# Kernel tuning notes

Hardware: AMD Instinct MI355X
Metric: run time of the kernel (lower is better)

Reference implementation:

```python
import jax, jax.numpy as jnp
import numpy as np

N = 12                      # input_size / Cholesky matrix dim
TRI = N * (N + 1) // 2      # 78 = MLP output size (lower-tri element count)
LW = 32                     # layer_width (hardcoded in source)
BATCH = 262144


def setup_inputs() -> dict:
    key = jax.random.key(0)
    ks = jax.random.split(key, 7)
    s = lambda fan_in: 1.0 / np.sqrt(fan_in)  # torch Linear default init scale
    return {
        "x":  jax.random.normal(ks[0], (BATCH, N), dtype=jnp.float32),
        "W1": jax.random.uniform(ks[1], (4 * LW, N),   minval=-s(N),      maxval=s(N),      dtype=jnp.float32),
        "b1": jax.random.uniform(ks[2], (4 * LW,),     minval=-s(N),      maxval=s(N),      dtype=jnp.float32),
        "W2": jax.random.uniform(ks[3], (LW, 4 * LW),  minval=-s(4 * LW), maxval=s(4 * LW), dtype=jnp.float32),
        "b2": jax.random.uniform(ks[4], (LW,),         minval=-s(4 * LW), maxval=s(4 * LW), dtype=jnp.float32),
        "W3": jax.random.uniform(ks[5], (TRI, LW),     minval=-s(LW),     maxval=s(LW),     dtype=jnp.float32),
        "b3": jax.random.uniform(ks[6], (TRI,),        minval=-s(LW),     maxval=s(LW),     dtype=jnp.float32),
    }


def reference(x, W1, b1, W2, b2, W3, b3):
    # MLP: Linear -> ELU -> Linear -> ELU -> Linear -> Softplus
    h = jax.nn.elu(x @ W1.T + b1)
    h = jax.nn.elu(h @ W2.T + b2)
    v = jax.nn.softplus(h @ W3.T + b3)          # [B, TRI]
    # Scatter tri elements into lower triangle, row-major (i>=j) order,
    # matching the source's nested i,j loop == jnp.tril_indices ordering.
    rows, cols = jnp.tril_indices(N)
    B = v.shape[0]
    L = jnp.zeros((B, N, N), dtype=v.dtype).at[:, rows, cols].set(v)
    # M @ M^T (batched), SPD output
    return jnp.einsum("bij,bkj->bik", L, L)
```

## Files before the change

kernel.cpp:

```cpp
#include <hip/hip_runtime.h>
#include <math.h>


namespace {

constexpr int ND  = 12;
constexpr int TRI = 78;
constexpr int BLK = 256;
constexpr int SPB = 512;

constexpr int oW3    = 0;
constexpr int oB3    = 2496;
constexpr int oW1    = 2576;
constexpr int oB1    = 4112;
constexpr int oW2T   = 4240;
constexpr int oB2    = 8336;
constexpr int oStage = 2576;
constexpr int STRIDE = 148;
constexpr int LDSF   = oStage + 64 * STRIDE;

__device__ __forceinline__ float elu_f(float v) {
    return v > 0.0f ? v : __expf(v) - 1.0f;
}
__device__ __forceinline__ float softplus_f(float v) {
    return fmaxf(v, 0.0f) + __logf(1.0f + __expf(-fabsf(v)));
}

__global__ __launch_bounds__(BLK, 2) void qnc(
    const float* __restrict__ x,
    const float* __restrict__ W1, const float* __restrict__ b1,
    const float* __restrict__ W2, const float* __restrict__ b2,
    const float* __restrict__ W3, const float* __restrict__ b3,
    float* __restrict__ out)
{
    __shared__ float lds[LDSF];
    const int t = threadIdx.x;

    for (int i = t; i < 2496; i += BLK) lds[oW3 + i] = W3[i];
    for (int i = t; i < 78;   i += BLK) lds[oB3 + i] = b3[i];
    for (int i = t; i < 1536; i += BLK) lds[oW1 + i] = W1[i];
    for (int i = t; i < 128;  i += BLK) lds[oB1 + i] = b1[i];
    for (int i = t; i < 4096; i += BLK) lds[oW2T + i] = W2[(i & 31) * 128 + (i >> 5)];
    for (int i = t; i < 32;   i += BLK) lds[oB2 + i] = b2[i];
    __syncthreads();

    const long sbase = (long)blockIdx.x * SPB;

    float xv0[ND], xv1[ND];
    {
        const float4* p0 = (const float4*)(x + (sbase + t) * ND);
        const float4* p1 = (const float4*)(x + (sbase + 256 + t) * ND);
        float4 a, b, c;
        a = p0[0]; b = p0[1]; c = p0[2];
        xv0[0]=a.x; xv0[1]=a.y; xv0[2]=a.z; xv0[3]=a.w;
        xv0[4]=b.x; xv0[5]=b.y; xv0[6]=b.z; xv0[7]=b.w;
        xv0[8]=c.x; xv0[9]=c.y; xv0[10]=c.z; xv0[11]=c.w;
        a = p1[0]; b = p1[1]; c = p1[2];
        xv1[0]=a.x; xv1[1]=a.y; xv1[2]=a.z; xv1[3]=a.w;
        xv1[4]=b.x; xv1[5]=b.y; xv1[6]=b.z; xv1[7]=b.w;
        xv1[8]=c.x; xv1[9]=c.y; xv1[10]=c.z; xv1[11]=c.w;
    }

    float h20[32], h21[32];
    #pragma unroll
    for (int k = 0; k < 32; ++k) { h20[k] = 0.0f; h21[k] = 0.0f; }

    #pragma unroll 2
    for (int j = 0; j < 128; ++j) {
        const float4 wa = *(const float4*)&lds[oW1 + j*12];
        const float4 wb = *(const float4*)&lds[oW1 + j*12 + 4];
        const float4 wc = *(const float4*)&lds[oW1 + j*12 + 8];
        const float bj = lds[oB1 + j];

        float p0 = fmaf(xv0[0], wa.x, bj);
        float p1 = xv0[1] * wa.y;
        float p2 = xv0[2] * wa.z;
        float p3 = xv0[3] * wa.w;
        p0 = fmaf(xv0[4], wb.x, p0); p1 = fmaf(xv0[5], wb.y, p1);
        p2 = fmaf(xv0[6], wb.z, p2); p3 = fmaf(xv0[7], wb.w, p3);
        p0 = fmaf(xv0[8], wc.x, p0); p1 = fmaf(xv0[9], wc.y, p1);
        p2 = fmaf(xv0[10], wc.z, p2); p3 = fmaf(xv0[11], wc.w, p3);
        const float e0 = elu_f((p0 + p1) + (p2 + p3));

        float q0 = fmaf(xv1[0], wa.x, bj);
        float q1 = xv1[1] * wa.y;
        float q2 = xv1[2] * wa.z;
        float q3 = xv1[3] * wa.w;
        q0 = fmaf(xv1[4], wb.x, q0); q1 = fmaf(xv1[5], wb.y, q1);
        q2 = fmaf(xv1[6], wb.z, q2); q3 = fmaf(xv1[7], wb.w, q3);
        q0 = fmaf(xv1[8], wc.x, q0); q1 = fmaf(xv1[9], wc.y, q1);
        q2 = fmaf(xv1[10], wc.z, q2); q3 = fmaf(xv1[11], wc.w, q3);
        const float e1 = elu_f((q0 + q1) + (q2 + q3));

        const float4* w2r = (const float4*)&lds[oW2T + j*32];
        #pragma unroll
        for (int kk = 0; kk < 8; ++kk) {
            const float4 w = w2r[kk];
            h20[4*kk+0] = fmaf(e0, w.x, h20[4*kk+0]);
            h20[4*kk+1] = fmaf(e0, w.y, h20[4*kk+1]);
            h20[4*kk+2] = fmaf(e0, w.z, h20[4*kk+2]);
            h20[4*kk+3] = fmaf(e0, w.w, h20[4*kk+3]);
            h21[4*kk+0] = fmaf(e1, w.x, h21[4*kk+0]);
            h21[4*kk+1] = fmaf(e1, w.y, h21[4*kk+1]);
            h21[4*kk+2] = fmaf(e1, w.z, h21[4*kk+2]);
            h21[4*kk+3] = fmaf(e1, w.w, h21[4*kk+3]);
        }
    }
    #pragma unroll
    for (int k = 0; k < 32; ++k) {
        const float bk = lds[oB2 + k];
        h20[k] = elu_f(h20[k] + bk);
        h21[k] = elu_f(h21[k] + bk);
    }

    __syncthreads();

    const int wv = t >> 6, lane = t & 63;
    float* sg = &lds[oStage + lane * STRIDE];

    auto phaseB = [&](const float (&h2)[32], int moff) {
        float L[TRI];
        #pragma unroll
        for (int tt = 0; tt < TRI; ++tt) {
            const float4* w = (const float4*)&lds[oW3 + tt*32];
            float a0 = lds[oB3 + tt], a1 = 0.f, a2 = 0.f, a3 = 0.f;
            #pragma unroll
            for (int q = 0; q < 8; ++q) {
                const float4 wq = w[q];
                a0 = fmaf(h2[4*q+0], wq.x, a0);
                a1 = fmaf(h2[4*q+1], wq.y, a1);
                a2 = fmaf(h2[4*q+2], wq.z, a2);
                a3 = fmaf(h2[4*q+3], wq.w, a3);
            }
            L[tt] = softplus_f((a0 + a1) + (a2 + a3));
        }

        for (int p = 0; p < 4; ++p) {
            if (wv == p) {
                #pragma unroll
                for (int i = 0; i < ND; ++i) {
                    float r[ND];
                    #pragma unroll
                    for (int k = 0; k < ND; ++k) {
                        const int mm = (i < k) ? i : k;
                        float s0 = 0.f, s1 = 0.f;
                        #pragma unroll
                        for (int j2 = 0; j2 <= mm; ++j2) {
                            const float pr = L[i*(i+1)/2 + j2] * L[k*(k+1)/2 + j2];
                            if (j2 & 1) s1 += pr; else s0 += pr;
                        }
                        r[k] = s0 + s1;
                    }
                    float4* sp = (float4*)(sg + i * ND);
                    sp[0] = make_float4(r[0], r[1], r[2],  r[3]);
                    sp[1] = make_float4(r[4], r[5], r[6],  r[7]);
                    sp[2] = make_float4(r[8], r[9], r[10], r[11]);
                }
            }
            __syncthreads();
            float4* g4 = (float4*)(out + (sbase + moff + p * 64) * 144);
            for (int u = t; u < 2304; u += BLK) {
                const int s = u / 36, q = u - s * 36;
                g4[u] = *(const float4*)&lds[oStage + s * STRIDE + q * 4];
            }
            __syncthreads();
        }
    };

    phaseB(h20, 0);
    phaseB(h21, 256);
}

}

extern "C" void kernel_launch(void* const* d_in, const int* in_sizes, int n_in,
                              void* d_out, int out_size, void* d_ws, size_t ws_size,
                              hipStream_t stream) {
    const float* x  = (const float*)d_in[0];
    const float* W1 = (const float*)d_in[1];
    const float* b1 = (const float*)d_in[2];
    const float* W2 = (const float*)d_in[3];
    const float* b2 = (const float*)d_in[4];
    const float* W3 = (const float*)d_in[5];
    const float* b3 = (const float*)d_in[6];
    float* out = (float*)d_out;

    const int batch  = in_sizes[0] / ND;
    const int blocks = batch / SPB;

    qnc<<<blocks, BLK, 0, stream>>>(x, W1, b1, W2, b2, W3, b3, out);
}
```

Measured before the change: 260.4 us.

## Run MLP layers on MFMA with split-fp16 emulation and parallel Gram rows

Moves all three linear layers from scalar FP32 FMAs to 16x16x32 fp16 MFMA instructions. FP32 precision is approximated with a hi/lo fp16 split and three MFMAs per product. Weights are pre-swizzled into MFMA fragment layout in LDS. The L·Lᵀ product is now split across 4 lane groups, each computing 3 rows, and samples per block drop to 256. The goal is to offload the compute-bound MLP to the matrix cores, at the cost of extra conversion work, a larger LDS footprint that may limit occupancy, and a small loss of accuracy.

```diff
diff --git a/kernel.cpp b/kernel.cpp
--- a/kernel.cpp
+++ b/kernel.cpp
@@ -5,25 +5,57 @@
 namespace {
 
 constexpr int ND  = 12;
-constexpr int TRI = 78;
 constexpr int BLK = 256;
-constexpr int SPB = 512;
-
-constexpr int oW3    = 0;
-constexpr int oB3    = 2496;
-constexpr int oW1    = 2576;
-constexpr int oB1    = 4112;
-constexpr int oW2T   = 4240;
-constexpr int oB2    = 8336;
-constexpr int oStage = 2576;
+constexpr int SPB = 256;
+
+typedef __attribute__((ext_vector_type(8))) _Float16 h8t;
+typedef __attribute__((ext_vector_type(4))) float    f4t;
+
+union FragU { h8t v; _Float16 s[8]; unsigned u[4]; };
+
+constexpr int oW1h = 0;
+constexpr int oW1l = 4096;
+constexpr int oW2h = 8192;
+constexpr int oW2l = 16384;
+constexpr int oW3h = 24576;
+constexpr int oW3l = 29696;
+constexpr int oB1B = 34816;
+constexpr int oB2B = 35328;
+constexpr int oB3B = 35456;
+constexpr int oStgB = 35776;
+constexpr int LDSB  = 73664;
+
+constexpr int oB1F = oB1B / 4, oB2F = oB2B / 4, oB3F = oB3B / 4;
+constexpr int oStgF = oStgB / 4;
 constexpr int STRIDE = 148;
-constexpr int LDSF   = oStage + 64 * STRIDE;
 
 __device__ __forceinline__ float elu_f(float v) {
     return v > 0.0f ? v : __expf(v) - 1.0f;
 }
 __device__ __forceinline__ float softplus_f(float v) {
     return fmaxf(v, 0.0f) + __logf(1.0f + __expf(-fabsf(v)));
+}
+
+template<int I0>
+__device__ __forceinline__ void gRows(const float (&L)[80], float* dst) {
+    #pragma unroll
+    for (int i = I0; i < I0 + 3; ++i) {
+        float r[12];
+        #pragma unroll
+        for (int k = 0; k < 12; ++k) {
+            const int mm = (i < k) ? i : k;
+            float s0 = 0.f, s1 = 0.f;
+            #pragma unroll
+            for (int j = 0; j <= mm; ++j) {
+                const float pr = L[i*(i+1)/2 + j] * L[k*(k+1)/2 + j];
+                if (j & 1) s1 += pr; else s0 += pr;
+            }
+            r[k] = s0 + s1;
+        }
+        *(f4t*)(dst + i*12 + 0) = (f4t){r[0], r[1], r[2],  r[3]};
+        *(f4t*)(dst + i*12 + 4) = (f4t){r[4], r[5], r[6],  r[7]};
+        *(f4t*)(dst + i*12 + 8) = (f4t){r[8], r[9], r[10], r[11]};
+    }
 }
 
 __global__ __launch_bounds__(BLK, 2) void qnc(
@@ -33,142 +65,189 @@
     const float* __restrict__ W3, const float* __restrict__ b3,
     float* __restrict__ out)
 {
-    __shared__ float lds[LDSF];
+    __shared__ __align__(16) unsigned char ldsB[LDSB];
+    float*     ldsF = (float*)ldsB;
+    _Float16*  sW1h = (_Float16*)(ldsB + oW1h);
+    _Float16*  sW1l = (_Float16*)(ldsB + oW1l);
+    _Float16*  sW2h = (_Float16*)(ldsB + oW2h);
+    _Float16*  sW2l = (_Float16*)(ldsB + oW2l);
+    _Float16*  sW3h = (_Float16*)(ldsB + oW3h);
+    _Float16*  sW3l = (_Float16*)(ldsB + oW3l);
+
     const int t = threadIdx.x;
-
-    for (int i = t; i < 2496; i += BLK) lds[oW3 + i] = W3[i];
-    for (int i = t; i < 78;   i += BLK) lds[oB3 + i] = b3[i];
-    for (int i = t; i < 1536; i += BLK) lds[oW1 + i] = W1[i];
-    for (int i = t; i < 128;  i += BLK) lds[oB1 + i] = b1[i];
-    for (int i = t; i < 4096; i += BLK) lds[oW2T + i] = W2[(i & 31) * 128 + (i >> 5)];
-    for (int i = t; i < 32;   i += BLK) lds[oB2 + i] = b2[i];
+    const int lane = t & 63, w = t >> 6;
+    const int sIn = lane & 15, h = lane >> 4;
+    const int sbase = blockIdx.x * SPB;
+
+    for (int i = t; i < 2048; i += BLK) {
+        const int m = i >> 8, l = (i >> 2) & 63, j = i & 3;
+        const int row = 16*m + (l & 15), k = 4*(l >> 4) + j;
+        const float v = (k < ND) ? W1[row*ND + k] : 0.0f;
+        const _Float16 hi = (_Float16)v;
+        sW1h[i] = hi;
+        sW1l[i] = (_Float16)(v - (float)hi);
+    }
+    for (int i = t; i < 4096; i += BLK) {
+        const int t2 = i >> 9, l = (i >> 3) & 63, j = i & 7;
+        const int kt = t2 >> 1, mt = t2 & 1, hq = l >> 4;
+        const int row = 16*mt + (l & 15);
+        const int k = 32*kt + ((j < 4) ? 4*hq + j : 16 + 4*hq + (j - 4));
+        const float v = W2[row*128 + k];
+        const _Float16 hi = (_Float16)v;
+        sW2h[i] = hi;
+        sW2l[i] = (_Float16)(v - (float)hi);
+    }
+    for (int i = t; i < 2560; i += BLK) {
+        const int mt = i >> 9, l = (i >> 3) & 63, j = i & 7;
+        const int hq = l >> 4;
+        const int row = 16*mt + (l & 15);
+        const int k = (j < 4) ? 4*hq + j : 16 + 4*hq + (j - 4);
+        const float v = (row < 78) ? W3[row*32 + k] : 0.0f;
+        const _Float16 hi = (_Float16)v;
+        sW3h[i] = hi;
+        sW3l[i] = (_Float16)(v - (float)hi);
+    }
+    for (int i = t; i < 128; i += BLK) ldsF[oB1F + i] = b1[i];
+    for (int i = t; i < 32;  i += BLK) ldsF[oB2F + i] = b2[i];
+    for (int i = t; i < 80;  i += BLK) ldsF[oB3F + i] = (i < 78) ? b3[i] : 0.0f;
+
+    {
+        const float4* xg = (const float4*)(x + (long)sbase * ND);
+        float4* xs = (float4*)(ldsB + oStgB);
+        for (int i = t; i < 768; i += BLK) xs[i] = xg[i];
+    }
     __syncthreads();
 
-    const long sbase = (long)blockIdx.x * SPB;
-
-    float xv0[ND], xv1[ND];
-    {
-        const float4* p0 = (const float4*)(x + (sbase + t) * ND);
-        const float4* p1 = (const float4*)(x + (sbase + 256 + t) * ND);
-        float4 a, b, c;
-        a = p0[0]; b = p0[1]; c = p0[2];
-        xv0[0]=a.x; xv0[1]=a.y; xv0[2]=a.z; xv0[3]=a.w;
-        xv0[4]=b.x; xv0[5]=b.y; xv0[6]=b.z; xv0[7]=b.w;
-        xv0[8]=c.x; xv0[9]=c.y; xv0[10]=c.z; xv0[11]=c.w;
-        a = p1[0]; b = p1[1]; c = p1[2];
-        xv1[0]=a.x; xv1[1]=a.y; xv1[2]=a.z; xv1[3]=a.w;
-        xv1[4]=b.x; xv1[5]=b.y; xv1[6]=b.z; xv1[7]=b.w;
-        xv1[8]=c.x; xv1[9]=c.y; xv1[10]=c.z; xv1[11]=c.w;
-    }
-
-    float h20[32], h21[32];
+    unsigned B1h[4][2], B1l[4][2];
     #pragma unroll
-    for (int k = 0; k < 32; ++k) { h20[k] = 0.0f; h21[k] = 0.0f; }
-
-    #pragma unroll 2
-    for (int j = 0; j < 128; ++j) {
-        const float4 wa = *(const float4*)&lds[oW1 + j*12];
-        const float4 wb = *(const float4*)&lds[oW1 + j*12 + 4];
-        const float4 wc = *(const float4*)&lds[oW1 + j*12 + 8];
-        const float bj = lds[oB1 + j];
-
-        float p0 = fmaf(xv0[0], wa.x, bj);
-        float p1 = xv0[1] * wa.y;
-        float p2 = xv0[2] * wa.z;
-        float p3 = xv0[3] * wa.w;
-        p0 = fmaf(xv0[4], wb.x, p0); p1 = fmaf(xv0[5], wb.y, p1);
-        p2 = fmaf(xv0[6], wb.z, p2); p3 = fmaf(xv0[7], wb.w, p3);
-        p0 = fmaf(xv0[8], wc.x, p0); p1 = fmaf(xv0[9], wc.y, p1);
-        p2 = fmaf(xv0[10], wc.z, p2); p3 = fmaf(xv0[11], wc.w, p3);
-        const float e0 = elu_f((p0 + p1) + (p2 + p3));
-
-        float q0 = fmaf(xv1[0], wa.x, bj);
-        float q1 = xv1[1] * wa.y;
-        float q2 = xv1[2] * wa.z;
-        float q3 = xv1[3] * wa.w;
-        q0 = fmaf(xv1[4], wb.x, q0); q1 = fmaf(xv1[5], wb.y, q1);
-        q2 = fmaf(xv1[6], wb.z, q2); q3 = fmaf(xv1[7], wb.w, q3);
-        q0 = fmaf(xv1[8], wc.x, q0); q1 = fmaf(xv1[9], wc.y, q1);
-        q2 = fmaf(xv1[10], wc.z, q2); q3 = fmaf(xv1[11], wc.w, q3);
-        const float e1 = elu_f((q0 + q1) + (q2 + q3));
-
-        const float4* w2r = (const float4*)&lds[oW2T + j*32];
-        #pragma unroll
-        for (int kk = 0; kk < 8; ++kk) {
-            const float4 w = w2r[kk];
-            h20[4*kk+0] = fmaf(e0, w.x, h20[4*kk+0]);
-            h20[4*kk+1] = fmaf(e0, w.y, h20[4*kk+1]);
-            h20[4*kk+2] = fmaf(e0, w.z, h20[4*kk+2]);
-            h20[4*kk+3] = fmaf(e0, w.w, h20[4*kk+3]);
-            h21[4*kk+0] = fmaf(e1, w.x, h21[4*kk+0]);
-            h21[4*kk+1] = fmaf(e1, w.y, h21[4*kk+1]);
-            h21[4*kk+2] = fmaf(e1, w.z, h21[4*kk+2]);
-            h21[4*kk+3] = fmaf(e1, w.w, h21[4*kk+3]);
-        }
-    }
-    #pragma unroll
-    for (int k = 0; k < 32; ++k) {
-        const float bk = lds[oB2 + k];
-        h20[k] = elu_f(h20[k] + bk);
-        h21[k] = elu_f(h21[k] + bk);
-    }
-
+    for (int g = 0; g < 4; ++g) {
+        float xv[4] = {0.f, 0.f, 0.f, 0.f};
+        if (h < 3) {
+            const float4 q = *(const float4*)(ldsF + oStgF + (g*64 + w*16 + sIn)*ND + 4*h);
+            xv[0] = q.x; xv[1] = q.y; xv[2] = q.z; xv[3] = q.w;
+        }
+        FragU bh, bl;
+        #pragma unroll
+        for (int j = 0; j < 4; ++j) {
+            const _Float16 hi = (_Float16)xv[j];
+            bh.s[j] = hi;
+            bl.s[j] = (_Float16)(xv[j] - (float)hi);
+        }
+        B1h[g][0] = bh.u[0]; B1h[g][1] = bh.u[1];
+        B1l[g][0] = bl.u[0]; B1l[g][1] = bl.u[1];
+    }
     __syncthreads();
 
-    const int wv = t >> 6, lane = t & 63;
-    float* sg = &lds[oStage + lane * STRIDE];
-
-    auto phaseB = [&](const float (&h2)[32], int moff) {
-        float L[TRI];
-        #pragma unroll
-        for (int tt = 0; tt < TRI; ++tt) {
-            const float4* w = (const float4*)&lds[oW3 + tt*32];
-            float a0 = lds[oB3 + tt], a1 = 0.f, a2 = 0.f, a3 = 0.f;
+    for (int g = 0; g < 4; ++g) {
+        unsigned xh0 = 0, xh1 = 0, xl0 = 0, xl1 = 0;
+        #pragma unroll
+        for (int gg = 0; gg < 4; ++gg)
+            if (gg == g) { xh0 = B1h[gg][0]; xh1 = B1h[gg][1];
+                           xl0 = B1l[gg][0]; xl1 = B1l[gg][1]; }
+        FragU bh; bh.u[0] = xh0; bh.u[1] = xh1; bh.u[2] = 0; bh.u[3] = 0;
+        FragU bl; bl.u[0] = xl0; bl.u[1] = xl1; bl.u[2] = 0; bl.u[3] = 0;
+
+        f4t d1[8];
+        #pragma unroll
+        for (int m = 0; m < 8; ++m) {
+            f4t c = *(const f4t*)(ldsF + oB1F + 16*m + 4*h);
+            FragU Ah, Al;
+            { const uint2 p = *(const uint2*)(ldsB + oW1h + (m*64 + lane)*8);
+              Ah.u[0] = p.x; Ah.u[1] = p.y; Ah.u[2] = 0; Ah.u[3] = 0; }
+            { const uint2 p = *(const uint2*)(ldsB + oW1l + (m*64 + lane)*8);
+              Al.u[0] = p.x; Al.u[1] = p.y; Al.u[2] = 0; Al.u[3] = 0; }
+            c = __builtin_amdgcn_mfma_f32_16x16x32_f16(Ah.v, bh.v, c, 0, 0, 0);
+            c = __builtin_amdgcn_mfma_f32_16x16x32_f16(Ah.v, bl.v, c, 0, 0, 0);
+            d1[m] = __builtin_amdgcn_mfma_f32_16x16x32_f16(Al.v, bh.v, c, 0, 0, 0);
+        }
+
+        FragU b2h[4], b2l[4];
+        #pragma unroll
+        for (int kt = 0; kt < 4; ++kt) {
             #pragma unroll
-            for (int q = 0; q < 8; ++q) {
-                const float4 wq = w[q];
-                a0 = fmaf(h2[4*q+0], wq.x, a0);
-                a1 = fmaf(h2[4*q+1], wq.y, a1);
-                a2 = fmaf(h2[4*q+2], wq.z, a2);
-                a3 = fmaf(h2[4*q+3], wq.w, a3);
+            for (int r = 0; r < 4; ++r) {
+                const float e0 = elu_f(d1[2*kt][r]);
+                const float e1 = elu_f(d1[2*kt + 1][r]);
+                const _Float16 h0 = (_Float16)e0;
+                const _Float16 h1 = (_Float16)e1;
+                b2h[kt].s[r]     = h0;
+                b2l[kt].s[r]     = (_Float16)(e0 - (float)h0);
+                b2h[kt].s[4 + r] = h1;
+                b2l[kt].s[4 + r] = (_Float16)(e1 - (float)h1);
             }
-            L[tt] = softplus_f((a0 + a1) + (a2 + a3));
-        }
-
-        for (int p = 0; p < 4; ++p) {
-            if (wv == p) {
-                #pragma unroll
-                for (int i = 0; i < ND; ++i) {
-                    float r[ND];
-                    #pragma unroll
-                    for (int k = 0; k < ND; ++k) {
-                        const int mm = (i < k) ? i : k;
-                        float s0 = 0.f, s1 = 0.f;
-                        #pragma unroll
-                        for (int j2 = 0; j2 <= mm; ++j2) {
-                            const float pr = L[i*(i+1)/2 + j2] * L[k*(k+1)/2 + j2];
-                            if (j2 & 1) s1 += pr; else s0 += pr;
-                        }
-                        r[k] = s0 + s1;
-                    }
-                    float4* sp = (float4*)(sg + i * ND);
-                    sp[0] = make_float4(r[0], r[1], r[2],  r[3]);
-                    sp[1] = make_float4(r[4], r[5], r[6],  r[7]);
-                    sp[2] = make_float4(r[8], r[9], r[10], r[11]);
-                }
+        }
+
+        f4t a2m[2], a2c[2];
+        #pragma unroll
+        for (int mt = 0; mt < 2; ++mt) {
+            a2m[mt] = *(const f4t*)(ldsF + oB2F + 16*mt + 4*h);
+            a2c[mt] = (f4t){0.f, 0.f, 0.f, 0.f};
+        }
+        #pragma unroll
+        for (int kt = 0; kt < 4; ++kt) {
+            #pragma unroll
+            for (int mt = 0; mt < 2; ++mt) {
+                const int t2 = kt*2 + mt;
+                FragU Ah, Al;
+                Ah.v = *(const h8t*)(ldsB + oW2h + (t2*64 + lane)*16);
+                Al.v = *(const h8t*)(ldsB + oW2l + (t2*64 + lane)*16);
+                a2m[mt] = __builtin_amdgcn_mfma_f32_16x16x32_f16(Ah.v, b2h[kt].v, a2m[mt], 0, 0, 0);
+                a2c[mt] = __builtin_amdgcn_mfma_f32_16x16x32_f16(Ah.v, b2l[kt].v, a2c[mt], 0, 0, 0);
+                a2c[mt] = __builtin_amdgcn_mfma_f32_16x16x32_f16(Al.v, b2h[kt].v, a2c[mt], 0, 0, 0);
             }
-            __syncthreads();
-            float4* g4 = (float4*)(out + (sbase + moff + p * 64) * 144);
-            for (int u = t; u < 2304; u += BLK) {
-                const int s = u / 36, q = u - s * 36;
-                g4[u] = *(const float4*)&lds[oStage + s * STRIDE + q * 4];
-            }
-            __syncthreads();
-        }
-    };
-
-    phaseB(h20, 0);
-    phaseB(h21, 256);
+        }
+
+        FragU b3hF, b3lF;
+        #pragma unroll
+        for (int r = 0; r < 4; ++r) {
+            const float e0 = elu_f(a2m[0][r] + a2c[0][r]);
+            const float e1 = elu_f(a2m[1][r] + a2c[1][r]);
+            const _Float16 h0 = (_Float16)e0;
+            const _Float16 h1 = (_Float16)e1;
+            b3hF.s[r]     = h0;
+            b3lF.s[r]     = (_Float16)(e0 - (float)h0);
+            b3hF.s[4 + r] = h1;
+            b3lF.s[4 + r] = (_Float16)(e1 - (float)h1);
+        }
+
+        float* Lw = ldsF + oStgF + w*2368;
+        #pragma unroll
+        for (int mt = 0; mt < 5; ++mt) {
+            f4t c = *(const f4t*)(ldsF + oB3F + 16*mt + 4*h);
+            FragU Ah, Al;
+            Ah.v = *(const h8t*)(ldsB + oW3h + (mt*64 + lane)*16);
+            Al.v = *(const h8t*)(ldsB + oW3l + (mt*64 + lane)*16);
+            c = __builtin_amdgcn_mfma_f32_16x16x32_f16(Ah.v, b3hF.v, c, 0, 0, 0);
+            c = __builtin_amdgcn_mfma_f32_16x16x32_f16(Ah.v, b3lF.v, c, 0, 0, 0);
+            c = __builtin_amdgcn_mfma_f32_16x16x32_f16(Al.v, b3hF.v, c, 0, 0, 0);
+            f4t s;
+            s[0] = softplus_f(c[0]); s[1] = softplus_f(c[1]);
+            s[2] = softplus_f(c[2]); s[3] = softplus_f(c[3]);
+            *(f4t*)(Lw + sIn*84 + 16*mt + 4*h) = s;
+        }
+
+        float L[80];
+        #pragma unroll
+        for (int jq = 0; jq < 20; ++jq) {
+            const f4t q = *(const f4t*)(Lw + sIn*84 + 4*jq);
+            L[4*jq + 0] = q[0]; L[4*jq + 1] = q[1];
+            L[4*jq + 2] = q[2]; L[4*jq + 3] = q[3];
+        }
+
+        float* stg = ldsF + oStgF + (w*16 + sIn) * STRIDE;
+        if      (h == 0) gRows<0>(L, stg);
+        else if (h == 1) gRows<3>(L, stg);
+        else if (h == 2) gRows<6>(L, stg);
+        else             gRows<9>(L, stg);
+
+        __syncthreads();
+        float4* g4 = (float4*)(out + (long)(sbase + g*64) * 144);
+        for (int u = t; u < 2304; u += BLK) {
+            const int s = u / 36, q = u - s * 36;
+            g4[u] = *(const float4*)(ldsF + oStgF + s * STRIDE + q * 4);
+        }
+        __syncthreads();
+    }
 }
 
 }
```

Result: faster. 223.8 us, median of 3 (-14.1%).
